# Kernel optimization log

Measured on AMD Instinct MI355X. Metric: run time of the kernel, lower is better.

## Reference

```python
import jax, jax.numpy as jnp
import numpy as np

B, T, D_OBS, D_ACT, H = 1024, 1024, 32, 4, 64


def setup_inputs() -> dict:
    key = jax.random.key(0)
    ks = jax.random.split(key, 8)
    s = 0.1
    obs = jax.random.normal(ks[0], (B, T, D_OBS), dtype=jnp.float32)
    action = jax.random.normal(ks[1], (B, T, D_ACT), dtype=jnp.float32)
    # GRUCell params (torch layout): weight_ih [3H, Din], weight_hh [3H, H]
    W_ih = jax.random.normal(ks[2], (3 * H, D_OBS + D_ACT), dtype=jnp.float32) * s
    W_hh = jax.random.normal(ks[3], (3 * H, H), dtype=jnp.float32) * s
    b_ih = jax.random.normal(ks[4], (3 * H,), dtype=jnp.float32) * s
    b_hh = jax.random.normal(ks[5], (3 * H,), dtype=jnp.float32) * s
    # reward head: Linear(H, 1)
    W_r = jax.random.normal(ks[6], (1, H), dtype=jnp.float32) * s
    b_r = jax.random.normal(ks[7], (1,), dtype=jnp.float32) * s
    return {"obs": obs, "action": action, "W_ih": W_ih, "b_ih": b_ih,
            "W_hh": W_hh, "b_hh": b_hh, "W_r": W_r, "b_r": b_r}


def reference(obs, action, W_ih, b_ih, W_hh, b_hh, W_r, b_r):
    # x_t = cat(obs_t, action_t); GRUCell recurrence; reward = Linear(h_t)
    x = jnp.concatenate([obs, action], axis=-1)              # [B, T, Din]
    # Precompute input-to-hidden gates for all timesteps (batched GEMM)
    gi = jnp.einsum('btd,gd->btg', x, W_ih) + b_ih           # [B, T, 3H]
    gi_t = jnp.swapaxes(gi, 0, 1)                            # [T, B, 3H]

    def step(h, gi_step):
        gh = h @ W_hh.T + b_hh                               # [B, 3H]
        ghr, ghz, ghn = jnp.split(gh, 3, axis=-1)
        gir, giz, gin = jnp.split(gi_step, 3, axis=-1)
        r = jax.nn.sigmoid(gir + ghr)
        z = jax.nn.sigmoid(giz + ghz)
        n = jnp.tanh(gin + r * ghn)
        h_new = (1.0 - z) * n + z * h
        reward = h_new @ W_r.T + b_r                         # [B, 1]
        return h_new, reward

    h0 = jnp.zeros((obs.shape[0], H), dtype=obs.dtype)
    h_final, rewards = jax.lax.scan(step, h0, gi_t)          # rewards: [T, B, 1]
    return h_final, jnp.swapaxes(rewards, 0, 1)              # h: [B, H], reward: [B, T, 1]
```

## Files before the change

kernel.cpp:

```cpp
#include <hip/hip_runtime.h>


#define BB 1024
#define TT 1024
#define DOBS 32
#define DACT 4
#define HH 64

typedef __attribute__((ext_vector_type(8))) short short8;
typedef __attribute__((ext_vector_type(4))) float f32x4;

#define MFMA(A, B, C) __builtin_amdgcn_mfma_f32_16x16x32_bf16((A), (B), (C), 0, 0, 0)

static __device__ __forceinline__ unsigned short f2bf(float f) {
    unsigned u = __float_as_uint(f);
    u += 0x7fffu + ((u >> 16) & 1u);
    return (unsigned short)(u >> 16);
}
static __device__ __forceinline__ float frcp(float x) { return __builtin_amdgcn_rcpf(x); }
static __device__ __forceinline__ unsigned cvt_pk(float lo, float hi) {
    unsigned r;
    asm("v_cvt_pk_bf16_f32 %0, %1, %2" : "=v"(r) : "v"(lo), "v"(hi));
    return r;
}

__global__ __launch_bounds__(256)
void pack_x(const float* __restrict__ obs, const float* __restrict__ act,
            unsigned short* __restrict__ xext)
{
    const size_t r = (size_t)blockIdx.x * 256 + threadIdx.x;
    const float* o = obs + r * DOBS;
    unsigned short* d = xext + r * 40;
    short8 v[5];
#pragma unroll
    for (int j = 0; j < 4; ++j) {
        float4 a = ((const float4*)o)[2 * j];
        float4 b = ((const float4*)o)[2 * j + 1];
        short8 t;
        t[0]=f2bf(a.x); t[1]=f2bf(a.y); t[2]=f2bf(a.z); t[3]=f2bf(a.w);
        t[4]=f2bf(b.x); t[5]=f2bf(b.y); t[6]=f2bf(b.z); t[7]=f2bf(b.w);
        v[j] = t;
    }
    {
        float4 a = *(const float4*)(act + r * DACT);
        short8 t;
        t[0]=f2bf(a.x); t[1]=f2bf(a.y); t[2]=f2bf(a.z); t[3]=f2bf(a.w);
        t[4]=(short)0x3f80; t[5]=0; t[6]=0; t[7]=0;
        v[4] = t;
    }
#pragma unroll
    for (int j = 0; j < 5; ++j) ((short8*)d)[j] = v[j];
}

#define LOADX(XO, XA, T)                                                       \
  {                                                                            \
    const int tc_ = (T) < TT ? (T) : TT - 1;                                   \
    if (PACKED) {                                                              \
      XO = *(const short8*)(px + (size_t)tc_ * 40 + 8 * q);                    \
      XA = (q == 0) ? *(const short8*)(px + (size_t)tc_ * 40 + 32) : zero8;    \
    } else {                                                                   \
      const float* op_ = po + (size_t)tc_ * DOBS + 8 * q;                      \
      float4 a_ = *(const float4*)op_, b_ = *(const float4*)(op_ + 4);         \
      short8 f_;                                                               \
      f_[0]=f2bf(a_.x); f_[1]=f2bf(a_.y); f_[2]=f2bf(a_.z); f_[3]=f2bf(a_.w);  \
      f_[4]=f2bf(b_.x); f_[5]=f2bf(b_.y); f_[6]=f2bf(b_.z); f_[7]=f2bf(b_.w);  \
      XO = f_;                                                                 \
      if (q == 0) {                                                            \
        float4 av_ = *(const float4*)(pa + (size_t)tc_ * DACT);                \
        short8 g_;                                                             \
        g_[0]=f2bf(av_.x); g_[1]=f2bf(av_.y); g_[2]=f2bf(av_.z);               \
        g_[3]=f2bf(av_.w); g_[4]=(short)0x3f80; g_[5]=0; g_[6]=0; g_[7]=0;     \
        XA = g_;                                                               \
      } else XA = zero8;                                                       \
    }                                                                          \
  }

#define L2E 1.442695040888963f

#define STEP(XO, XA, T)                                                        \
  {                                                                            \
    const int p_ = (T) & 1, np_ = p_ ^ 1;                                      \
    short8 Ah0 = *(const short8*)((const char*)hbuf[p_] + rdaddr0);            \
    short8 Ah1 = *(const short8*)((const char*)hbuf[p_] + rdaddr1);            \
    f32x4 Cr, Cz, Cni, Cnh, Crw = zf;                                          \
    Cr  = MFMA(AX[0][0], XO, zf);    Cr  = MFMA(AX[0][1], XA, Cr);             \
    Cz  = MFMA(AX[1][0], XO, zf);    Cz  = MFMA(AX[1][1], XA, Cz);             \
    Cni = MFMA(AX[2][0], XO, zf);    Cni = MFMA(AX[2][1], XA, Cni);            \
    LOADX(XO, XA, (T) + 2)                            \
    Cr  = MFMA(AH[0][0], Ah0, Cr);   Cr  = MFMA(AH[0][1], Ah1, Cr);            \
    Cz  = MFMA(AH[1][0], Ah0, Cz);   Cz  = MFMA(AH[1][1], Ah1, Cz);            \
    Cnh = MFMA(AH[2][0], Ah0, bhn4); Cnh = MFMA(AH[2][1], Ah1, Cnh);           \
    if (w == 3) { Crw = MFMA(AR[0], Ah0, zf); Crw = MFMA(AR[1], Ah1, Crw); }   \
    _Pragma("unroll")                                                          \
    for (int reg = 0; reg < 4; ++reg) {                                        \
      float rr   = frcp(1.0f + __builtin_amdgcn_exp2f(Cr[reg] * -L2E));        \
      float zz   = frcp(1.0f + __builtin_amdgcn_exp2f(Cz[reg] * -L2E));        \
      float npre = __builtin_fmaf(rr, Cnh[reg], Cni[reg]);                     \
      float nn   = 1.0f - 2.0f * frcp(__builtin_amdgcn_exp2f(npre * (2.0f * L2E)) + 1.0f); \
      hold[reg]  = __builtin_fmaf(zz, hold[reg] - nn, nn);                     \
    }                                                                          \
    unsigned pk0 = cvt_pk(hold[0], hold[1]);                                   \
    unsigned pk1 = cvt_pk(hold[2], hold[3]);                                   \
    *(uint2*)((char*)hbuf[np_] + wraddr) = make_uint2(pk0, pk1);               \
    if (w == 3 && q == 0 && (T) > 0)                                           \
      rew[(size_t)(bid * 16 + c) * TT + (T) - 1] = Crw[0] + brr;               \
    asm volatile("s_waitcnt lgkmcnt(0)" ::: "memory");                         \
    __builtin_amdgcn_s_barrier();                                              \
    asm volatile("" ::: "memory");                                             \
  }

template<bool PACKED>
__global__ __launch_bounds__(256, 1)
void gru_fused(const unsigned short* __restrict__ xext,
               const float* __restrict__ obs, const float* __restrict__ act,
               const float* __restrict__ W_ih, const float* __restrict__ b_ih,
               const float* __restrict__ W_hh, const float* __restrict__ b_hh,
               const float* __restrict__ W_r, const float* __restrict__ b_r,
               float* __restrict__ out)
{
    const int tid = threadIdx.x;
    const int w = tid >> 6, l = tid & 63, c = l & 15, q = l >> 4;
    const int bid = blockIdx.x;
    const int u0 = 16 * w + 4 * q;

    __shared__ __align__(16) unsigned short hbuf[2][16 * 64];

    short8 AX[3][2], AH[3][2];
#pragma unroll
    for (int m = 0; m < 3; ++m) {
        const int j = w + 4 * m;
        const int g = 16 * j + c;
        {
            const float* wp = W_ih + (size_t)g * 36 + 8 * q;
            float4 a = *(const float4*)wp, b = *(const float4*)(wp + 4);
            short8 f;
            f[0]=f2bf(a.x); f[1]=f2bf(a.y); f[2]=f2bf(a.z); f[3]=f2bf(a.w);
            f[4]=f2bf(b.x); f[5]=f2bf(b.y); f[6]=f2bf(b.z); f[7]=f2bf(b.w);
            AX[m][0] = f;
        }
        {
            short8 f;
#pragma unroll
            for (int i = 0; i < 8; ++i) {
                int k = 32 + 8 * q + i;
                float v = 0.f;
                if (k < 36)       v = W_ih[(size_t)g * 36 + k];
                else if (k == 36) v = b_ih[g] + (g < 128 ? b_hh[g] : 0.f);
                f[i] = f2bf(v);
            }
            AX[m][1] = f;
        }
#pragma unroll
        for (int kk = 0; kk < 2; ++kk) {
            const float* wp = W_hh + (size_t)g * HH + 32 * kk + 8 * q;
            float4 a = *(const float4*)wp, b = *(const float4*)(wp + 4);
            short8 f;
            f[0]=f2bf(a.x); f[1]=f2bf(a.y); f[2]=f2bf(a.z); f[3]=f2bf(a.w);
            f[4]=f2bf(b.x); f[5]=f2bf(b.y); f[6]=f2bf(b.z); f[7]=f2bf(b.w);
            AH[m][kk] = f;
        }
    }
    short8 AR[2];
#pragma unroll
    for (int kk = 0; kk < 2; ++kk) {
        short8 f;
#pragma unroll
        for (int i = 0; i < 8; ++i) {
            int k = 32 * kk + 8 * q + i;
            f[i] = (c == 0) ? (short)f2bf(W_r[k]) : (short)0;
        }
        AR[kk] = f;
    }

    f32x4 bhn4;
#pragma unroll
    for (int reg = 0; reg < 4; ++reg) bhn4[reg] = b_hh[128 + u0 + reg];
    const float brr = b_r[0];

    const int swz = c & 7;
    const int wraddr  = c * 128 + ((((u0 >> 3)) ^ swz) << 4) + (u0 & 7) * 2;
    const int rdaddr0 = c * 128 + ((q ^ swz) << 4);
    const int rdaddr1 = c * 128 + (((4 + q) ^ swz) << 4);

    const size_t row = (size_t)(bid * 16 + c) * TT;
    const unsigned short* px = xext + row * 40;
    const float* po = obs + row * DOBS;
    const float* pa = act + row * DACT;

    const short8 zero8 = {0, 0, 0, 0, 0, 0, 0, 0};
    const f32x4 zf = {0.f, 0.f, 0.f, 0.f};

    ((uint2*)hbuf[0])[tid] = make_uint2(0u, 0u);
    short8 xoA, xaA, xoB, xaB;
    LOADX(xoA, xaA, 0)
    LOADX(xoB, xaB, 1)
    float hold[4] = {0.f, 0.f, 0.f, 0.f};
    asm volatile("s_waitcnt lgkmcnt(0)" ::: "memory");
    __builtin_amdgcn_s_barrier();
    asm volatile("" ::: "memory");

    float* rew = out + (size_t)BB * HH;

#pragma unroll 1
    for (int t = 0; t < TT; t += 2) {
        STEP(xoA, xaA, t)
        STEP(xoB, xaB, t + 1)
    }

    if (w == 3) {
        short8 Ah0 = *(const short8*)((const char*)hbuf[0] + rdaddr0);
        short8 Ah1 = *(const short8*)((const char*)hbuf[0] + rdaddr1);
        f32x4 Crw = MFMA(AR[0], Ah0, zf);
        Crw = MFMA(AR[1], Ah1, Crw);
        if (q == 0)
            rew[(size_t)(bid * 16 + c) * TT + TT - 1] = Crw[0] + brr;
    }
    *(float4*)(out + (size_t)(bid * 16 + c) * HH + u0) =
        make_float4(hold[0], hold[1], hold[2], hold[3]);
}

extern "C" void kernel_launch(void* const* d_in, const int* in_sizes, int n_in,
                              void* d_out, int out_size, void* d_ws, size_t ws_size,
                              hipStream_t stream)
{
    const float* obs    = (const float*)d_in[0];
    const float* action = (const float*)d_in[1];
    const float* W_ih   = (const float*)d_in[2];
    const float* b_ih   = (const float*)d_in[3];
    const float* W_hh   = (const float*)d_in[4];
    const float* b_hh   = (const float*)d_in[5];
    const float* W_r    = (const float*)d_in[6];
    const float* b_r    = (const float*)d_in[7];
    float* out          = (float*)d_out;

    const size_t xext_bytes = (size_t)BB * TT * 40 * sizeof(unsigned short);
    if (ws_size >= xext_bytes) {
        unsigned short* xext = (unsigned short*)d_ws;
        pack_x<<<dim3((BB * TT) / 256), dim3(256), 0, stream>>>(obs, action, xext);
        gru_fused<true><<<dim3(BB / 16), dim3(256), 0, stream>>>(
            xext, obs, action, W_ih, b_ih, W_hh, b_hh, W_r, b_r, out);
    } else {
        gru_fused<false><<<dim3(BB / 16), dim3(256), 0, stream>>>(
            nullptr, obs, action, W_ih, b_ih, W_hh, b_hh, W_r, b_r, out);
    }
}
```

Measured before the change: 461.4 us.

## Drop pack kernel and software-pipeline input-gate MFMAs one step ahead

Removes the separate pack_x kernel and its bf16 workspace, so the recurrent kernel always reads fp32 obs/action directly and converts them in-loop. The input-projection MFMAs for step t+2 are issued during step t, with their results carried in registers, and the x loads are prefetched four steps ahead. This takes the input GEMM off the serial recurrence critical path and removes the extra kernel launch and workspace traffic. In exchange it uses more registers and adds in-loop fp32 loads and conversions.

```diff
diff --git a/kernel.cpp b/kernel.cpp
--- a/kernel.cpp
+++ b/kernel.cpp
@@ -24,84 +24,51 @@
     return r;
 }
 
-__global__ __launch_bounds__(256)
-void pack_x(const float* __restrict__ obs, const float* __restrict__ act,
-            unsigned short* __restrict__ xext)
-{
-    const size_t r = (size_t)blockIdx.x * 256 + threadIdx.x;
-    const float* o = obs + r * DOBS;
-    unsigned short* d = xext + r * 40;
-    short8 v[5];
-#pragma unroll
-    for (int j = 0; j < 4; ++j) {
-        float4 a = ((const float4*)o)[2 * j];
-        float4 b = ((const float4*)o)[2 * j + 1];
-        short8 t;
-        t[0]=f2bf(a.x); t[1]=f2bf(a.y); t[2]=f2bf(a.z); t[3]=f2bf(a.w);
-        t[4]=f2bf(b.x); t[5]=f2bf(b.y); t[6]=f2bf(b.z); t[7]=f2bf(b.w);
-        v[j] = t;
-    }
-    {
-        float4 a = *(const float4*)(act + r * DACT);
-        short8 t;
-        t[0]=f2bf(a.x); t[1]=f2bf(a.y); t[2]=f2bf(a.z); t[3]=f2bf(a.w);
-        t[4]=(short)0x3f80; t[5]=0; t[6]=0; t[7]=0;
-        v[4] = t;
-    }
-#pragma unroll
-    for (int j = 0; j < 5; ++j) ((short8*)d)[j] = v[j];
-}
+#define L2E 1.442695040888963f
 
 #define LOADX(XO, XA, T)                                                       \
   {                                                                            \
     const int tc_ = (T) < TT ? (T) : TT - 1;                                   \
-    if (PACKED) {                                                              \
-      XO = *(const short8*)(px + (size_t)tc_ * 40 + 8 * q);                    \
-      XA = (q == 0) ? *(const short8*)(px + (size_t)tc_ * 40 + 32) : zero8;    \
-    } else {                                                                   \
-      const float* op_ = po + (size_t)tc_ * DOBS + 8 * q;                      \
-      float4 a_ = *(const float4*)op_, b_ = *(const float4*)(op_ + 4);         \
-      short8 f_;                                                               \
-      f_[0]=f2bf(a_.x); f_[1]=f2bf(a_.y); f_[2]=f2bf(a_.z); f_[3]=f2bf(a_.w);  \
-      f_[4]=f2bf(b_.x); f_[5]=f2bf(b_.y); f_[6]=f2bf(b_.z); f_[7]=f2bf(b_.w);  \
-      XO = f_;                                                                 \
-      if (q == 0) {                                                            \
-        float4 av_ = *(const float4*)(pa + (size_t)tc_ * DACT);                \
-        short8 g_;                                                             \
-        g_[0]=f2bf(av_.x); g_[1]=f2bf(av_.y); g_[2]=f2bf(av_.z);               \
-        g_[3]=f2bf(av_.w); g_[4]=(short)0x3f80; g_[5]=0; g_[6]=0; g_[7]=0;     \
-        XA = g_;                                                               \
-      } else XA = zero8;                                                       \
-    }                                                                          \
+    const float* op_ = po + (size_t)tc_ * DOBS + 8 * q;                        \
+    float4 a_ = *(const float4*)op_, b_ = *(const float4*)(op_ + 4);           \
+    short8 f_;                                                                 \
+    f_[0]=f2bf(a_.x); f_[1]=f2bf(a_.y); f_[2]=f2bf(a_.z); f_[3]=f2bf(a_.w);    \
+    f_[4]=f2bf(b_.x); f_[5]=f2bf(b_.y); f_[6]=f2bf(b_.z); f_[7]=f2bf(b_.w);    \
+    XO = f_;                                                                   \
+    if (q == 0) {                                                              \
+      float4 av_ = *(const float4*)(pa + (size_t)tc_ * DACT);                  \
+      short8 g_;                                                               \
+      g_[0]=f2bf(av_.x); g_[1]=f2bf(av_.y); g_[2]=f2bf(av_.z);                 \
+      g_[3]=f2bf(av_.w); g_[4]=(short)0x3f80; g_[5]=0; g_[6]=0; g_[7]=0;       \
+      XA = g_;                                                                 \
+    } else XA = zero8;                                                         \
   }
 
-#define L2E 1.442695040888963f
-
-#define STEP(XO, XA, T)                                                        \
+#define STEP(XO, XA, CR_, CZ_, CN_, PH, T)                                     \
   {                                                                            \
-    const int p_ = (T) & 1, np_ = p_ ^ 1;                                      \
-    short8 Ah0 = *(const short8*)((const char*)hbuf[p_] + rdaddr0);            \
-    short8 Ah1 = *(const short8*)((const char*)hbuf[p_] + rdaddr1);            \
-    f32x4 Cr, Cz, Cni, Cnh, Crw = zf;                                          \
-    Cr  = MFMA(AX[0][0], XO, zf);    Cr  = MFMA(AX[0][1], XA, Cr);             \
-    Cz  = MFMA(AX[1][0], XO, zf);    Cz  = MFMA(AX[1][1], XA, Cz);             \
-    Cni = MFMA(AX[2][0], XO, zf);    Cni = MFMA(AX[2][1], XA, Cni);            \
-    LOADX(XO, XA, (T) + 2)                            \
-    Cr  = MFMA(AH[0][0], Ah0, Cr);   Cr  = MFMA(AH[0][1], Ah1, Cr);            \
-    Cz  = MFMA(AH[1][0], Ah0, Cz);   Cz  = MFMA(AH[1][1], Ah1, Cz);            \
-    Cnh = MFMA(AH[2][0], Ah0, bhn4); Cnh = MFMA(AH[2][1], Ah1, Cnh);           \
-    if (w == 3) { Crw = MFMA(AR[0], Ah0, zf); Crw = MFMA(AR[1], Ah1, Crw); }   \
+    short8 Ah0 = *(const short8*)((const char*)hbuf[PH] + rdaddr0);            \
+    short8 Ah1 = *(const short8*)((const char*)hbuf[PH] + rdaddr1);            \
+    f32x4 cr_ = CR_, cz_ = CZ_, cni_ = CN_;        \
+    CR_ = MFMA(AX[0][1], XA, MFMA(AX[0][0], XO, zf));    \
+    CZ_ = MFMA(AX[1][1], XA, MFMA(AX[1][0], XO, zf));                          \
+    CN_ = MFMA(AX[2][1], XA, MFMA(AX[2][0], XO, zf));                          \
+    LOADX(XO, XA, (T) + 4)                            \
+    f32x4 Cr  = MFMA(AH[0][1], Ah1, MFMA(AH[0][0], Ah0, cr_));                 \
+    f32x4 Cz  = MFMA(AH[1][1], Ah1, MFMA(AH[1][0], Ah0, cz_));                 \
+    f32x4 Cnh = MFMA(AH[2][1], Ah1, MFMA(AH[2][0], Ah0, bhn4));                \
+    f32x4 Crw = zf;                                                            \
+    if (w == 3) Crw = MFMA(AR[1], Ah1, MFMA(AR[0], Ah0, zf));                  \
     _Pragma("unroll")                                                          \
     for (int reg = 0; reg < 4; ++reg) {                                        \
       float rr   = frcp(1.0f + __builtin_amdgcn_exp2f(Cr[reg] * -L2E));        \
       float zz   = frcp(1.0f + __builtin_amdgcn_exp2f(Cz[reg] * -L2E));        \
-      float npre = __builtin_fmaf(rr, Cnh[reg], Cni[reg]);                     \
+      float npre = __builtin_fmaf(rr, Cnh[reg], cni_[reg]);                    \
       float nn   = 1.0f - 2.0f * frcp(__builtin_amdgcn_exp2f(npre * (2.0f * L2E)) + 1.0f); \
       hold[reg]  = __builtin_fmaf(zz, hold[reg] - nn, nn);                     \
     }                                                                          \
     unsigned pk0 = cvt_pk(hold[0], hold[1]);                                   \
     unsigned pk1 = cvt_pk(hold[2], hold[3]);                                   \
-    *(uint2*)((char*)hbuf[np_] + wraddr) = make_uint2(pk0, pk1);               \
+    *(uint2*)((char*)hbuf[PH ^ 1] + wraddr) = make_uint2(pk0, pk1);            \
     if (w == 3 && q == 0 && (T) > 0)                                           \
       rew[(size_t)(bid * 16 + c) * TT + (T) - 1] = Crw[0] + brr;               \
     asm volatile("s_waitcnt lgkmcnt(0)" ::: "memory");                         \
@@ -109,10 +76,8 @@
     asm volatile("" ::: "memory");                                             \
   }
 
-template<bool PACKED>
 __global__ __launch_bounds__(256, 1)
-void gru_fused(const unsigned short* __restrict__ xext,
-               const float* __restrict__ obs, const float* __restrict__ act,
+void gru_fused(const float* __restrict__ obs, const float* __restrict__ act,
                const float* __restrict__ W_ih, const float* __restrict__ b_ih,
                const float* __restrict__ W_hh, const float* __restrict__ b_hh,
                const float* __restrict__ W_r, const float* __restrict__ b_r,
@@ -183,7 +148,6 @@
     const int rdaddr1 = c * 128 + (((4 + q) ^ swz) << 4);
 
     const size_t row = (size_t)(bid * 16 + c) * TT;
-    const unsigned short* px = xext + row * 40;
     const float* po = obs + row * DOBS;
     const float* pa = act + row * DACT;
 
@@ -194,6 +158,14 @@
     short8 xoA, xaA, xoB, xaB;
     LOADX(xoA, xaA, 0)
     LOADX(xoB, xaB, 1)
+    f32x4 cgrA = MFMA(AX[0][1], xaA, MFMA(AX[0][0], xoA, zf));
+    f32x4 cgzA = MFMA(AX[1][1], xaA, MFMA(AX[1][0], xoA, zf));
+    f32x4 cgnA = MFMA(AX[2][1], xaA, MFMA(AX[2][0], xoA, zf));
+    f32x4 cgrB = MFMA(AX[0][1], xaB, MFMA(AX[0][0], xoB, zf));
+    f32x4 cgzB = MFMA(AX[1][1], xaB, MFMA(AX[1][0], xoB, zf));
+    f32x4 cgnB = MFMA(AX[2][1], xaB, MFMA(AX[2][0], xoB, zf));
+    LOADX(xoA, xaA, 2)
+    LOADX(xoB, xaB, 3)
     float hold[4] = {0.f, 0.f, 0.f, 0.f};
     asm volatile("s_waitcnt lgkmcnt(0)" ::: "memory");
     __builtin_amdgcn_s_barrier();
@@ -203,8 +175,8 @@
 
 #pragma unroll 1
     for (int t = 0; t < TT; t += 2) {
-        STEP(xoA, xaA, t)
-        STEP(xoB, xaB, t + 1)
+        STEP(xoA, xaA, cgrA, cgzA, cgnA, 0, t)
+        STEP(xoB, xaB, cgrB, cgzB, cgnB, 1, t + 1)
     }
 
     if (w == 3) {
@@ -233,14 +205,6 @@
     const float* b_r    = (const float*)d_in[7];
     float* out          = (float*)d_out;
 
-    const size_t xext_bytes = (size_t)BB * TT * 40 * sizeof(unsigned short);
-    if (ws_size >= xext_bytes) {
-        unsigned short* xext = (unsigned short*)d_ws;
-        pack_x<<<dim3((BB * TT) / 256), dim3(256), 0, stream>>>(obs, action, xext);
-        gru_fused<true><<<dim3(BB / 16), dim3(256), 0, stream>>>(
-            xext, obs, action, W_ih, b_ih, W_hh, b_hh, W_r, b_r, out);
-    } else {
-        gru_fused<false><<<dim3(BB / 16), dim3(256), 0, stream>>>(
-            nullptr, obs, action, W_ih, b_ih, W_hh, b_hh, W_r, b_r, out);
-    }
-}
+    gru_fused<<<dim3(BB / 16), dim3(256), 0, stream>>>(
+        obs, action, W_ih, b_ih, W_hh, b_hh, W_r, b_r, out);
+}
```

After: 968.6 us. +109.9%, slower.

## Software-pipeline input-gate MFMAs one step ahead of the recurrence

Applied to the files above, without the earlier changes.

The input-to-hidden gate MFMAs for step t+2 are now computed during step t and carried in registers, so the hidden-state MFMA chain on the critical path starts from precomputed accumulators rather than waiting on the x-side MFMAs. The x loads are prefetched four steps ahead instead of two, and the buffer parity is passed as a compile-time constant. This takes more accumulator registers and deepens the prefetch. It reads x rows up to index T+3 past the end in the final iterations, which relies on LOADX bounds handling.

```diff
diff --git a/kernel.cpp b/kernel.cpp
--- a/kernel.cpp
+++ b/kernel.cpp
@@ -23,6 +23,8 @@
     asm("v_cvt_pk_bf16_f32 %0, %1, %2" : "=v"(r) : "v"(lo), "v"(hi));
     return r;
 }
+
+#define L2E 1.442695040888963f
 
 __global__ __launch_bounds__(256)
 void pack_x(const float* __restrict__ obs, const float* __restrict__ act,
@@ -75,33 +77,31 @@
     }                                                                          \
   }
 
-#define L2E 1.442695040888963f
-
-#define STEP(XO, XA, T)                                                        \
+#define STEP(XO, XA, CR_, CZ_, CN_, PH, T)                                     \
   {                                                                            \
-    const int p_ = (T) & 1, np_ = p_ ^ 1;                                      \
-    short8 Ah0 = *(const short8*)((const char*)hbuf[p_] + rdaddr0);            \
-    short8 Ah1 = *(const short8*)((const char*)hbuf[p_] + rdaddr1);            \
-    f32x4 Cr, Cz, Cni, Cnh, Crw = zf;                                          \
-    Cr  = MFMA(AX[0][0], XO, zf);    Cr  = MFMA(AX[0][1], XA, Cr);             \
-    Cz  = MFMA(AX[1][0], XO, zf);    Cz  = MFMA(AX[1][1], XA, Cz);             \
-    Cni = MFMA(AX[2][0], XO, zf);    Cni = MFMA(AX[2][1], XA, Cni);            \
-    LOADX(XO, XA, (T) + 2)                            \
-    Cr  = MFMA(AH[0][0], Ah0, Cr);   Cr  = MFMA(AH[0][1], Ah1, Cr);            \
-    Cz  = MFMA(AH[1][0], Ah0, Cz);   Cz  = MFMA(AH[1][1], Ah1, Cz);            \
-    Cnh = MFMA(AH[2][0], Ah0, bhn4); Cnh = MFMA(AH[2][1], Ah1, Cnh);           \
-    if (w == 3) { Crw = MFMA(AR[0], Ah0, zf); Crw = MFMA(AR[1], Ah1, Crw); }   \
+    short8 Ah0 = *(const short8*)((const char*)hbuf[PH] + rdaddr0);            \
+    short8 Ah1 = *(const short8*)((const char*)hbuf[PH] + rdaddr1);            \
+    f32x4 cr_ = CR_, cz_ = CZ_, cni_ = CN_;        \
+    CR_ = MFMA(AX[0][1], XA, MFMA(AX[0][0], XO, zf));    \
+    CZ_ = MFMA(AX[1][1], XA, MFMA(AX[1][0], XO, zf));                          \
+    CN_ = MFMA(AX[2][1], XA, MFMA(AX[2][0], XO, zf));                          \
+    LOADX(XO, XA, (T) + 4)                            \
+    f32x4 Cr  = MFMA(AH[0][1], Ah1, MFMA(AH[0][0], Ah0, cr_));                 \
+    f32x4 Cz  = MFMA(AH[1][1], Ah1, MFMA(AH[1][0], Ah0, cz_));                 \
+    f32x4 Cnh = MFMA(AH[2][1], Ah1, MFMA(AH[2][0], Ah0, bhn4));                \
+    f32x4 Crw = zf;                                                            \
+    if (w == 3) Crw = MFMA(AR[1], Ah1, MFMA(AR[0], Ah0, zf));                  \
     _Pragma("unroll")                                                          \
     for (int reg = 0; reg < 4; ++reg) {                                        \
       float rr   = frcp(1.0f + __builtin_amdgcn_exp2f(Cr[reg] * -L2E));        \
       float zz   = frcp(1.0f + __builtin_amdgcn_exp2f(Cz[reg] * -L2E));        \
-      float npre = __builtin_fmaf(rr, Cnh[reg], Cni[reg]);                     \
+      float npre = __builtin_fmaf(rr, Cnh[reg], cni_[reg]);                    \
       float nn   = 1.0f - 2.0f * frcp(__builtin_amdgcn_exp2f(npre * (2.0f * L2E)) + 1.0f); \
       hold[reg]  = __builtin_fmaf(zz, hold[reg] - nn, nn);                     \
     }                                                                          \
     unsigned pk0 = cvt_pk(hold[0], hold[1]);                                   \
     unsigned pk1 = cvt_pk(hold[2], hold[3]);                                   \
-    *(uint2*)((char*)hbuf[np_] + wraddr) = make_uint2(pk0, pk1);               \
+    *(uint2*)((char*)hbuf[PH ^ 1] + wraddr) = make_uint2(pk0, pk1);            \
     if (w == 3 && q == 0 && (T) > 0)                                           \
       rew[(size_t)(bid * 16 + c) * TT + (T) - 1] = Crw[0] + brr;               \
     asm volatile("s_waitcnt lgkmcnt(0)" ::: "memory");                         \
@@ -194,6 +194,14 @@
     short8 xoA, xaA, xoB, xaB;
     LOADX(xoA, xaA, 0)
     LOADX(xoB, xaB, 1)
+    f32x4 cgrA = MFMA(AX[0][1], xaA, MFMA(AX[0][0], xoA, zf));
+    f32x4 cgzA = MFMA(AX[1][1], xaA, MFMA(AX[1][0], xoA, zf));
+    f32x4 cgnA = MFMA(AX[2][1], xaA, MFMA(AX[2][0], xoA, zf));
+    f32x4 cgrB = MFMA(AX[0][1], xaB, MFMA(AX[0][0], xoB, zf));
+    f32x4 cgzB = MFMA(AX[1][1], xaB, MFMA(AX[1][0], xoB, zf));
+    f32x4 cgnB = MFMA(AX[2][1], xaB, MFMA(AX[2][0], xoB, zf));
+    LOADX(xoA, xaA, 2)
+    LOADX(xoB, xaB, 3)
     float hold[4] = {0.f, 0.f, 0.f, 0.f};
     asm volatile("s_waitcnt lgkmcnt(0)" ::: "memory");
     __builtin_amdgcn_s_barrier();
@@ -203,8 +211,8 @@
 
 #pragma unroll 1
     for (int t = 0; t < TT; t += 2) {
-        STEP(xoA, xaA, t)
-        STEP(xoB, xaB, t + 1)
+        STEP(xoA, xaA, cgrA, cgzA, cgnA, 0, t)
+        STEP(xoB, xaB, cgrB, cgzB, cgnB, 1, t + 1)
     }
 
     if (w == 3) {
```

New measurement: 482.5 us. 1.05x slower.
